# Kernel tuning notes

Hardware: AMD Instinct MI355X
Metric: run time of the kernel (lower is better)

The kernel has to match this reference:

```python
import jax, jax.numpy as jnp
import numpy as np

B, S, D, H = 4, 2048, 768, 12
HD = D // H
EPS = 1e-5

def setup_inputs() -> dict:
    key = jax.random.key(0)
    ks = jax.random.split(key, 6)
    sc = 0.02
    return {
        "x": jax.random.normal(ks[0], (B, S, D), jnp.float32),
        "ln1_g": jnp.ones((D,), jnp.float32),
        "ln1_b": jnp.zeros((D,), jnp.float32),
        "W_qkv": jax.random.normal(ks[1], (D, 3 * D), jnp.float32) * sc,
        "b_qkv": jnp.zeros((3 * D,), jnp.float32),
        "W_o": jax.random.normal(ks[2], (D, D), jnp.float32) * sc,
        "b_o": jnp.zeros((D,), jnp.float32),
        "ln2_g": jnp.ones((D,), jnp.float32),
        "ln2_b": jnp.zeros((D,), jnp.float32),
        "W1": jax.random.normal(ks[3], (D, 4 * D), jnp.float32) * sc,
        "b1": jnp.zeros((4 * D,), jnp.float32),
        "W2": jax.random.normal(ks[4], (4 * D, D), jnp.float32) * sc,
        "b2": jnp.zeros((D,), jnp.float32),
    }

def _layernorm(x, g, b):
    mu = jnp.mean(x, axis=-1, keepdims=True)
    var = jnp.mean(jnp.square(x - mu), axis=-1, keepdims=True)
    return (x - mu) * jax.lax.rsqrt(var + EPS) * g + b

def _block(x, ln1_g, ln1_b, W_qkv, b_qkv, W_o, b_o, ln2_g, ln2_b, W1, b1, W2, b2):
    b, s, d = x.shape
    h = H
    # --- attention ---
    xn = _layernorm(x, ln1_g, ln1_b)
    qkv = xn @ W_qkv + b_qkv                      # [B,S,3D]
    q, k, v = jnp.split(qkv, 3, axis=-1)
    q = q.reshape(b, s, h, d // h).transpose(0, 2, 1, 3)  # [B,H,S,hd]
    k = k.reshape(b, s, h, d // h).transpose(0, 2, 1, 3)
    v = v.reshape(b, s, h, d // h).transpose(0, 2, 1, 3)
    # NOTE: faithful scale = 1/sqrt(embedding_dim), not head_dim
    scores = jnp.einsum('bhqd,bhkd->bhqk', q, k) / jnp.sqrt(jnp.float32(d))
    causal = jnp.tril(jnp.ones((s, s), bool))
    scores = jnp.where(causal[None, None], scores, -jnp.inf)
    attn = jax.nn.softmax(scores, axis=-1)
    ctx = jnp.einsum('bhqk,bhkd->bhqd', attn, v)  # [B,H,S,hd]
    ctx = ctx.transpose(0, 2, 1, 3).reshape(b, s, d)
    x = x + ctx @ W_o + b_o
    # --- MLP ---
    xn2 = _layernorm(x, ln2_g, ln2_b)
    hdn = jax.nn.gelu(xn2 @ W1 + b1, approximate=False)
    x = x + hdn @ W2 + b2
    return x

def reference(x, ln1_g, ln1_b, W_qkv, b_qkv, W_o, b_o, ln2_g, ln2_b, W1, b1, W2, b2):
    return _block(x, ln1_g, ln1_b, W_qkv, b_qkv, W_o, b_o, ln2_g, ln2_b, W1, b1, W2, b2)
```

## Files before the change

kernel.cpp:

```cpp
#include <hip/hip_runtime.h>
#include <math.h>

#define DIM   768
#define SEQ   2048
#define BATCH 4
#define NH    12
#define HD    64
#define ROWS  (BATCH*SEQ)
#define QKVW  (3*DIM)

typedef __bf16 bf16;
typedef __bf16 bf16x8 __attribute__((ext_vector_type(8)));
typedef float  f32x4  __attribute__((ext_vector_type(4)));

#define AS1 __attribute__((address_space(1)))
#define AS3 __attribute__((address_space(3)))

__device__ __forceinline__ void gload_lds16(const void* g, void* l) {
    __builtin_amdgcn_global_load_lds((const AS1 void*)g, (AS3 void*)l, 16, 0, 0);
}

#define QSCALE 0.05205877475f

__global__ __launch_bounds__(256) void ln_kernel(const float* __restrict__ x,
                                                 const float* __restrict__ g,
                                                 const float* __restrict__ beta,
                                                 bf16* __restrict__ out)
{
    __shared__ float red[8];
    const int row = blockIdx.x;
    const int tid = threadIdx.x;
    const int w = tid >> 6, lane = tid & 63;
    const float* xr = x + (size_t)row * DIM;

    const float v0 = xr[tid], v1 = xr[tid + 256], v2 = xr[tid + 512];
    float s  = v0 + v1 + v2;
    float s2 = v0*v0 + v1*v1 + v2*v2;
    #pragma unroll
    for (int m = 1; m < 64; m <<= 1) {
        s  += __shfl_xor(s,  m);
        s2 += __shfl_xor(s2, m);
    }
    if (lane == 0) { red[2*w] = s; red[2*w + 1] = s2; }
    __syncthreads();
    s  = red[0] + red[2] + red[4] + red[6];
    s2 = red[1] + red[3] + red[5] + red[7];
    const float mean = s * (1.0f / DIM);
    const float var  = s2 * (1.0f / DIM) - mean * mean;
    const float rstd = rsqrtf(var + 1e-5f);

    bf16* outr = out + (size_t)row * DIM;
    outr[tid]       = (bf16)((v0 - mean) * rstd * g[tid]       + beta[tid]);
    outr[tid + 256] = (bf16)((v1 - mean) * rstd * g[tid + 256] + beta[tid + 256]);
    outr[tid + 512] = (bf16)((v2 - mean) * rstd * g[tid + 512] + beta[tid + 512]);
}

__global__ __launch_bounds__(256) void transpose_cvt(const float* __restrict__ in,
                                                     bf16* __restrict__ out,
                                                     int K, int N)
{
    __shared__ float tile[32][33];
    const int n0 = blockIdx.x * 32, k0 = blockIdx.y * 32;
    const int tx = threadIdx.x, ty = threadIdx.y;
    #pragma unroll
    for (int j = 0; j < 4; j++)
        tile[ty + 8*j][tx] = in[(size_t)(k0 + ty + 8*j) * N + n0 + tx];
    __syncthreads();
    #pragma unroll
    for (int j = 0; j < 4; j++)
        out[(size_t)(n0 + ty + 8*j) * K + k0 + tx] = (bf16)tile[tx][ty + 8*j];
}

template<int MODE>
__global__ __launch_bounds__(256) void gemm_bf16(const bf16* __restrict__ A,
                                                 const bf16* __restrict__ Bt,
                                                 const float* __restrict__ bias,
                                                 const float* __restrict__ res,
                                                 void* __restrict__ Cout,
                                                 int M, int N, int K, int nx)
{
    __shared__ bf16 As[2][128 * 64];
    __shared__ bf16 Bs[2][128 * 64];

    const int nwg = gridDim.x;
    const int bid = blockIdx.x;
    const int id  = (bid & 7) * (nwg >> 3) + (bid >> 3);
    const int m0  = (id / nx) * 128;
    const int n0  = (id % nx) * 128;

    const int tid = threadIdx.x, lane = tid & 63, w = tid >> 6;
    const int wr = w >> 1, wc = w & 1;
    const int g = lane >> 4, lr = lane & 15;

    f32x4 acc[4][4];
    #pragma unroll
    for (int i = 0; i < 4; i++)
        #pragma unroll
        for (int j = 0; j < 4; j++) acc[i][j] = (f32x4){0.f, 0.f, 0.f, 0.f};

    const int srow = 32 * w + (lane >> 3);
    const int scol = ((lane & 7) ^ ((lane >> 3) & 7)) * 8;
    const bf16* Ag = A  + (size_t)(m0 + srow) * K + scol;
    const bf16* Bg = Bt + (size_t)(n0 + srow) * K + scol;
    const int woff = (32 * w) * 64;

    const int cx0 = ((0 + g) ^ (lr & 7)) * 8;
    const int cx1 = ((4 + g) ^ (lr & 7)) * 8;

    #pragma unroll
    for (int i = 0; i < 4; i++) {
        gload_lds16(Ag + (size_t)(8 * i) * K, &As[0][woff + i * 8 * 64]);
        gload_lds16(Bg + (size_t)(8 * i) * K, &Bs[0][woff + i * 8 * 64]);
    }
    __syncthreads();

    const int nk = K >> 6;
    for (int t = 0; t < nk; ++t) {
        const int c = t & 1;
        if (t + 1 < nk) {
            const int k0 = (t + 1) << 6;
            #pragma unroll
            for (int i = 0; i < 4; i++) {
                gload_lds16(Ag + (size_t)(8 * i) * K + k0, &As[c ^ 1][woff + i * 8 * 64]);
                gload_lds16(Bg + (size_t)(8 * i) * K + k0, &Bs[c ^ 1][woff + i * 8 * 64]);
            }
        }
        const bf16* Asl = As[c];
        const bf16* Bsl = Bs[c];
        #pragma unroll
        for (int ks = 0; ks < 2; ks++) {
            const int cx = ks ? cx1 : cx0;
            bf16x8 fa[4], fb[4];
            #pragma unroll
            for (int mi = 0; mi < 4; mi++)
                fa[mi] = *(const bf16x8*)(Asl + (64 * wr + 16 * mi + lr) * 64 + cx);
            #pragma unroll
            for (int nj = 0; nj < 4; nj++)
                fb[nj] = *(const bf16x8*)(Bsl + (64 * wc + 16 * nj + lr) * 64 + cx);
            #pragma unroll
            for (int mi = 0; mi < 4; mi++)
                #pragma unroll
                for (int nj = 0; nj < 4; nj++)
                    acc[mi][nj] = __builtin_amdgcn_mfma_f32_16x16x32_bf16(
                        fa[mi], fb[nj], acc[mi][nj], 0, 0, 0);
        }
        __syncthreads();
    }

    #pragma unroll
    for (int mi = 0; mi < 4; mi++) {
        #pragma unroll
        for (int r = 0; r < 4; r++) {
            const int row = m0 + 64 * wr + 16 * mi + 4 * g + r;
            #pragma unroll
            for (int nj = 0; nj < 4; nj++) {
                const int col = n0 + 64 * wc + 16 * nj + lr;
                float t = acc[mi][nj][r] + bias[col];
                if (MODE == 0) {
                    if (col < DIM) t *= QSCALE;
                    ((bf16*)Cout)[(size_t)row * N + col] = (bf16)t;
                } else if (MODE == 1) {
                    ((float*)Cout)[(size_t)row * N + col] = t + res[(size_t)row * N + col];
                } else {
                    t = 0.5f * t * (1.0f + erff(t * 0.70710678118654752f));
                    ((bf16*)Cout)[(size_t)row * N + col] = (bf16)t;
                }
            }
        }
    }
}

__global__ __launch_bounds__(256) void attn_mfma(const bf16* __restrict__ qkv,
                                                 bf16* __restrict__ ctx)
{
    __shared__ bf16 Ks[128 * 72];
    __shared__ bf16 Vt[64 * 136];
    __shared__ bf16 Ps[4 * 16 * 136];

    const int dd  = blockIdx.x;
    const int xcd = dd & 7;
    const int r_  = dd >> 3;
    const int p   = r_ & 15;
    const int G   = xcd + 8 * (r_ >> 4);
    const int h   = G % 12;
    const int b   = G / 12;

    const int tid = threadIdx.x, lane = tid & 63, w = tid >> 6;
    const int g = lane >> 4, lr = lane & 15;
    const size_t baserow = (size_t)b * SEQ;

    const int kr  = tid >> 1;
    const int d0s = (tid & 1) * 32;

    bf16x8 ones;
    #pragma unroll
    for (int j = 0; j < 8; j++) ones[j] = (bf16)1.0f;

    bf16x8 kreg[4], vreg[4];

    #pragma unroll
    for (int half = 0; half < 2; half++) {
        const int qt = half ? (31 - p) : p;

        bf16x8 qf[2];
        {
            const size_t qrow = baserow + qt * 64 + 16 * w + lr;
            const bf16* qp = qkv + qrow * QKVW + h * HD + g * 8;
            qf[0] = *(const bf16x8*)qp;
            qf[1] = *(const bf16x8*)(qp + 32);
        }

        f32x4 o[4], ol;
        #pragma unroll
        for (int nj = 0; nj < 4; nj++) o[nj] = (f32x4){0.f, 0.f, 0.f, 0.f};
        ol = (f32x4){0.f, 0.f, 0.f, 0.f};

        const int cmax = qt >> 1;

        {
            const bf16* kp = qkv + (baserow + kr) * QKVW + DIM + h * HD + d0s;
            const bf16* vp = qkv + (baserow + kr) * QKVW + 2 * DIM + h * HD + d0s;
            #pragma unroll
            for (int u = 0; u < 4; u++) kreg[u] = *(const bf16x8*)(kp + 8 * u);
            #pragma unroll
            for (int u = 0; u < 4; u++) vreg[u] = *(const bf16x8*)(vp + 8 * u);
        }

        for (int c = 0; c <= cmax; c++) {
            __syncthreads();
            {
                bf16* ksp = &Ks[kr * 72 + d0s];
                *(bf16x8*)(ksp + 0)  = kreg[0];
                *(bf16x8*)(ksp + 8)  = kreg[1];
                *(bf16x8*)(ksp + 16) = kreg[2];
                *(bf16x8*)(ksp + 24) = kreg[3];
            }
            {
                #pragma unroll
                for (int u = 0; u < 4; u++)
                    #pragma unroll
                    for (int j = 0; j < 8; j++)
                        Vt[(d0s + 8 * u + j) * 136 + kr] = vreg[u][j];
            }
            __syncthreads();

            if (c < cmax) {
                const bf16* kp = qkv + (baserow + (c + 1) * 128 + kr) * QKVW + DIM + h * HD + d0s;
                const bf16* vp = qkv + (baserow + (c + 1) * 128 + kr) * QKVW + 2 * DIM + h * HD + d0s;
                #pragma unroll
                for (int u = 0; u < 4; u++) kreg[u] = *(const bf16x8*)(kp + 8 * u);
                #pragma unroll
                for (int u = 0; u < 4; u++) vreg[u] = *(const bf16x8*)(vp + 8 * u);
            }

            f32x4 s[8];
            #pragma unroll
            for (int nj = 0; nj < 8; nj++) s[nj] = (f32x4){0.f, 0.f, 0.f, 0.f};
            __builtin_amdgcn_s_setprio(1);
            #pragma unroll
            for (int ks = 0; ks < 2; ks++) {
                #pragma unroll
                for (int nj = 0; nj < 8; nj++) {
                    const bf16x8 kf = *(const bf16x8*)&Ks[(16 * nj + lr) * 72 + ks * 32 + g * 8];
                    s[nj] = __builtin_amdgcn_mfma_f32_16x16x32_bf16(qf[ks], kf, s[nj], 0, 0, 0);
                }
            }
            __builtin_amdgcn_s_setprio(0);

            if (c == cmax) {
                const int qg = qt * 64 + 16 * w + 4 * g;
                #pragma unroll
                for (int nj = 0; nj < 8; nj++) {
                    const int kvg = c * 128 + 16 * nj + lr;
                    #pragma unroll
                    for (int r = 0; r < 4; r++)
                        if (kvg > qg + r) s[nj][r] = -INFINITY;
                }
            }

            bf16* pw = Ps + w * 16 * 136;
            #pragma unroll
            for (int nj = 0; nj < 8; nj++)
                #pragma unroll
                for (int r = 0; r < 4; r++)
                    pw[(4 * g + r) * 136 + 16 * nj + lr] = (bf16)exp2f(s[nj][r]);

            bf16x8 pf[4];
            #pragma unroll
            for (int ks = 0; ks < 4; ks++)
                pf[ks] = *(const bf16x8*)&pw[lr * 136 + ks * 32 + g * 8];
            __builtin_amdgcn_s_setprio(1);
            #pragma unroll
            for (int ks = 0; ks < 4; ks++) {
                #pragma unroll
                for (int nj = 0; nj < 4; nj++) {
                    const bf16x8 vf = *(const bf16x8*)&Vt[(16 * nj + lr) * 136 + ks * 32 + g * 8];
                    o[nj] = __builtin_amdgcn_mfma_f32_16x16x32_bf16(pf[ks], vf, o[nj], 0, 0, 0);
                }
                ol = __builtin_amdgcn_mfma_f32_16x16x32_bf16(pf[ks], ones, ol, 0, 0, 0);
            }
            __builtin_amdgcn_s_setprio(0);
        }

        #pragma unroll
        for (int r = 0; r < 4; r++) {
            const float inv = 1.0f / ol[r];
            const size_t row = baserow + qt * 64 + 16 * w + 4 * g + r;
            #pragma unroll
            for (int nj = 0; nj < 4; nj++)
                ctx[row * DIM + h * HD + 16 * nj + lr] = (bf16)(o[nj][r] * inv);
        }
    }
}

extern "C" void kernel_launch(void* const* d_in, const int* in_sizes, int n_in,
                              void* d_out, int out_size, void* d_ws, size_t ws_size,
                              hipStream_t stream)
{
    const float* x     = (const float*)d_in[0];
    const float* ln1_g = (const float*)d_in[1];
    const float* ln1_b = (const float*)d_in[2];
    const float* W_qkv = (const float*)d_in[3];
    const float* b_qkv = (const float*)d_in[4];
    const float* W_o   = (const float*)d_in[5];
    const float* b_o   = (const float*)d_in[6];
    const float* ln2_g = (const float*)d_in[7];
    const float* ln2_b = (const float*)d_in[8];
    const float* W1    = (const float*)d_in[9];
    const float* b1    = (const float*)d_in[10];
    const float* W2    = (const float*)d_in[11];
    const float* b2    = (const float*)d_in[12];
    float* out = (float*)d_out;

    char* wsb = (char*)d_ws;
    bf16*  xn     = (bf16*)(wsb);
    bf16*  qkvb   = (bf16*)(wsb + 12582912);
    bf16*  ctxb   = (bf16*)(wsb + 50331648);
    float* x1     = (float*)(wsb + 62914560);
    bf16*  hb     = (bf16*)(wsb + 88080384);
    bf16*  Wqkv_t = (bf16*)(wsb + 138412032);
    bf16*  Wo_t   = (bf16*)(wsb + 141950976);
    bf16*  W1_t   = (bf16*)(wsb + 143130624);
    bf16*  W2_t   = (bf16*)(wsb + 147849216);

    const dim3 tb(32, 8);
    transpose_cvt<<<dim3(QKVW / 32, DIM  / 32), tb, 0, stream>>>(W_qkv, Wqkv_t, DIM,  QKVW);
    transpose_cvt<<<dim3(DIM  / 32, DIM  / 32), tb, 0, stream>>>(W_o,   Wo_t,   DIM,  DIM);
    transpose_cvt<<<dim3(3072 / 32, DIM  / 32), tb, 0, stream>>>(W1,    W1_t,   DIM,  3072);
    transpose_cvt<<<dim3(DIM  / 32, 3072 / 32), tb, 0, stream>>>(W2,    W2_t,   3072, DIM);

    ln_kernel<<<ROWS, 256, 0, stream>>>(x, ln1_g, ln1_b, xn);
    gemm_bf16<0><<<(QKVW / 128) * (ROWS / 128), 256, 0, stream>>>(
        xn, Wqkv_t, b_qkv, nullptr, qkvb, ROWS, QKVW, DIM, QKVW / 128);
    attn_mfma<<<16 * NH * BATCH, 256, 0, stream>>>(qkvb, ctxb);
    gemm_bf16<1><<<(DIM / 128) * (ROWS / 128), 256, 0, stream>>>(
        ctxb, Wo_t, b_o, x, x1, ROWS, DIM, DIM, DIM / 128);
    ln_kernel<<<ROWS, 256, 0, stream>>>(x1, ln2_g, ln2_b, xn);
    gemm_bf16<2><<<(3072 / 128) * (ROWS / 128), 256, 0, stream>>>(
        xn, W1_t, b1, nullptr, hb, ROWS, 3072, DIM, 3072 / 128);
    gemm_bf16<1><<<(DIM / 128) * (ROWS / 128), 256, 0, stream>>>(
        hb, W2_t, b2, x1, out, ROWS, DIM, 3072, DIM / 128);
}
```

Before: 408.7 us.

## Overlap GEMM tile loads via partial vmcnt waits and vectorize epilogue with swapped MFMA operands

The GEMM main loop replaces the per-iteration __syncthreads with raw s_barrier plus an explicit s_waitcnt vmcnt(8). This lets the prefetch of the next K tile stay in flight while the current tile is consumed, and removes the separate prologue sync. The MFMA operands are swapped so each lane's accumulator holds four consecutive columns of one row. The epilogue can then use float4 bias and residual loads and 4-wide bf16 or float4 stores instead of scalar ones. It relies on correct vmcnt counting for the global_load_lds instructions, and a wrong count could cause races.

```diff
diff --git a/kernel.cpp b/kernel.cpp
--- a/kernel.cpp
+++ b/kernel.cpp
@@ -10,6 +10,7 @@
 #define QKVW  (3*DIM)
 
 typedef __bf16 bf16;
+typedef __bf16 bf16x4 __attribute__((ext_vector_type(4)));
 typedef __bf16 bf16x8 __attribute__((ext_vector_type(8)));
 typedef float  f32x4  __attribute__((ext_vector_type(4)));
 
@@ -109,22 +110,27 @@
 
     #pragma unroll
     for (int i = 0; i < 4; i++) {
-        gload_lds16(Ag + (size_t)(8 * i) * K, &As[0][woff + i * 8 * 64]);
-        gload_lds16(Bg + (size_t)(8 * i) * K, &Bs[0][woff + i * 8 * 64]);
-    }
-    __syncthreads();
+        gload_lds16(Ag + (size_t)(8 * i) * K, (void*)&As[0][woff + i * 8 * 64]);
+        gload_lds16(Bg + (size_t)(8 * i) * K, (void*)&Bs[0][woff + i * 8 * 64]);
+    }
 
     const int nk = K >> 6;
+    int c = 0;
     for (int t = 0; t < nk; ++t) {
-        const int c = t & 1;
+        if (t) __builtin_amdgcn_s_barrier();
         if (t + 1 < nk) {
             const int k0 = (t + 1) << 6;
             #pragma unroll
             for (int i = 0; i < 4; i++) {
-                gload_lds16(Ag + (size_t)(8 * i) * K + k0, &As[c ^ 1][woff + i * 8 * 64]);
-                gload_lds16(Bg + (size_t)(8 * i) * K + k0, &Bs[c ^ 1][woff + i * 8 * 64]);
-            }
-        }
+                gload_lds16(Ag + (size_t)(8 * i) * K + k0, (void*)&As[c ^ 1][woff + i * 8 * 64]);
+                gload_lds16(Bg + (size_t)(8 * i) * K + k0, (void*)&Bs[c ^ 1][woff + i * 8 * 64]);
+            }
+            asm volatile("s_waitcnt vmcnt(8)" ::: "memory");
+        } else {
+            asm volatile("s_waitcnt vmcnt(0)" ::: "memory");
+        }
+        __builtin_amdgcn_s_barrier();
+
         const bf16* Asl = As[c];
         const bf16* Bsl = Bs[c];
         #pragma unroll
@@ -142,29 +148,38 @@
                 #pragma unroll
                 for (int nj = 0; nj < 4; nj++)
                     acc[mi][nj] = __builtin_amdgcn_mfma_f32_16x16x32_bf16(
-                        fa[mi], fb[nj], acc[mi][nj], 0, 0, 0);
-        }
-        __syncthreads();
+                        fb[nj], fa[mi], acc[mi][nj], 0, 0, 0);
+        }
+        c ^= 1;
     }
 
     #pragma unroll
     for (int mi = 0; mi < 4; mi++) {
-        #pragma unroll
-        for (int r = 0; r < 4; r++) {
-            const int row = m0 + 64 * wr + 16 * mi + 4 * g + r;
-            #pragma unroll
-            for (int nj = 0; nj < 4; nj++) {
-                const int col = n0 + 64 * wc + 16 * nj + lr;
-                float t = acc[mi][nj][r] + bias[col];
-                if (MODE == 0) {
-                    if (col < DIM) t *= QSCALE;
-                    ((bf16*)Cout)[(size_t)row * N + col] = (bf16)t;
-                } else if (MODE == 1) {
-                    ((float*)Cout)[(size_t)row * N + col] = t + res[(size_t)row * N + col];
-                } else {
-                    t = 0.5f * t * (1.0f + erff(t * 0.70710678118654752f));
-                    ((bf16*)Cout)[(size_t)row * N + col] = (bf16)t;
-                }
+        const int row = m0 + 64 * wr + 16 * mi + lr;
+        #pragma unroll
+        for (int nj = 0; nj < 4; nj++) {
+            const int col0 = n0 + 64 * wc + 16 * nj + 4 * g;
+            const float4 bv = *(const float4*)&bias[col0];
+            float t0 = acc[mi][nj][0] + bv.x;
+            float t1 = acc[mi][nj][1] + bv.y;
+            float t2 = acc[mi][nj][2] + bv.z;
+            float t3 = acc[mi][nj][3] + bv.w;
+            if (MODE == 0) {
+                if (col0 < DIM) { t0 *= QSCALE; t1 *= QSCALE; t2 *= QSCALE; t3 *= QSCALE; }
+                bf16x4 o4 = {(bf16)t0, (bf16)t1, (bf16)t2, (bf16)t3};
+                *(bf16x4*)&((bf16*)Cout)[(size_t)row * N + col0] = o4;
+            } else if (MODE == 1) {
+                const float4 rv = *(const float4*)&res[(size_t)row * N + col0];
+                float4 ov;
+                ov.x = t0 + rv.x; ov.y = t1 + rv.y; ov.z = t2 + rv.z; ov.w = t3 + rv.w;
+                *(float4*)&((float*)Cout)[(size_t)row * N + col0] = ov;
+            } else {
+                t0 = 0.5f * t0 * (1.0f + erff(t0 * 0.70710678118654752f));
+                t1 = 0.5f * t1 * (1.0f + erff(t1 * 0.70710678118654752f));
+                t2 = 0.5f * t2 * (1.0f + erff(t2 * 0.70710678118654752f));
+                t3 = 0.5f * t3 * (1.0f + erff(t3 * 0.70710678118654752f));
+                bf16x4 o4 = {(bf16)t0, (bf16)t1, (bf16)t2, (bf16)t3};
+                *(bf16x4*)&((bf16*)Cout)[(size_t)row * N + col0] = o4;
             }
         }
     }
```

Result: slower. 422.8 us (+3.5%).
